# Optimization experiments

Measured on AMD Instinct MI355X. Metric: run time of the kernel, lower is better.

## Reference

```python
import jax, jax.numpy as jnp
import numpy as np

PAD_ID, SOS_ID, EOS_ID = 0, 1, 2


def setup_inputs() -> dict:
    key = jax.random.key(0)
    ks = jax.random.split(key, 8)
    V, E, H, B = 16000, 256, 512, 8
    s = 0.05  # weight scale to keep softmax well-conditioned
    return {
        "hidden": jax.random.normal(ks[0], (1, B, H), dtype=jnp.float32),
        "embedding": jax.random.normal(ks[1], (V, E), dtype=jnp.float32) * s,
        "w_ih": jax.random.normal(ks[2], (3 * H, E), dtype=jnp.float32) * s,
        "w_hh": jax.random.normal(ks[3], (3 * H, H), dtype=jnp.float32) * s,
        "b_ih": jax.random.normal(ks[4], (3 * H,), dtype=jnp.float32) * s,
        "b_hh": jax.random.normal(ks[5], (3 * H,), dtype=jnp.float32) * s,
        "w_out": jax.random.normal(ks[6], (V, H), dtype=jnp.float32) * s,
        "b_out": jax.random.normal(ks[7], (V,), dtype=jnp.float32) * s,
        "lenseq": 12,
        "k": 5,
    }


def reference(hidden, embedding, w_ih, w_hh, b_ih, b_hh, w_out, b_out, lenseq, k):
    V, E = embedding.shape
    _, B, H = hidden.shape
    dt = hidden.dtype
    pad_onehot = jax.nn.one_hot(PAD_ID, V, dtype=dt)

    def gru_cell(x_emb, h):  # x_emb: (k,B,E), h: (k,B,H); torch nn.GRU gate order r,z,n
        gi = x_emb @ w_ih.T + b_ih
        gh = h @ w_hh.T + b_hh
        i_r, i_z, i_n = jnp.split(gi, 3, axis=-1)
        h_r, h_z, h_n = jnp.split(gh, 3, axis=-1)
        r = jax.nn.sigmoid(i_r + h_r)
        z = jax.nn.sigmoid(i_z + h_z)
        n = jnp.tanh(i_n + r * h_n)
        return (1.0 - z) * n + z * h

    def step(carry, i):
        x, h, prob, res, _ = carry
        done = (x == EOS_ID) | (x == PAD_ID)            # (k,B)
        emb = embedding[x]                               # (k,B,E)
        h_new = gru_cell(emb, h)                         # (k,B,H)
        probs = jax.nn.softmax(h_new @ w_out.T + b_out, axis=-1)  # (k,B,V)
        pred = jnp.where(done[..., None], pad_onehot, probs)
        h = jnp.where(done[..., None], h, h_new)
        res = res.at[:, i].set(pred)                     # store raw pred (pre prob-scaling), as torch.cat copies
        scores = pred * prob[..., None]                  # (k,B,V); prob stays all-ones, faithful to source
        flat = scores.transpose(1, 0, 2).reshape(B, k * V)  # beam-major flatten per batch elem
        _, idx = jax.lax.top_k(flat, k)                  # (B,k)
        beam = (idx // V).T                              # (k,B)
        tok = (idx % V).T                                # (k,B)
        res = jnp.take_along_axis(res, beam[:, None, :, None], axis=0)
        prob = jnp.take_along_axis(prob, beam, axis=0)
        h = jnp.take_along_axis(h, beam[..., None], axis=0)
        return (tok, h, prob, res, pred), None

    x0 = jnp.full((k, B), SOS_ID, dtype=jnp.int32)
    h0 = jnp.broadcast_to(hidden[0], (k, B, H))
    prob0 = jnp.ones((k, B), dtype=dt)
    res0 = jnp.zeros((k, lenseq, B, V), dtype=dt)
    pred0 = jnp.zeros((k, B, V), dtype=dt)

    (x, h, prob, res, pred), _ = jax.lax.scan(step, (x0, h0, prob0, res0, pred0), jnp.arange(lenseq))

    # final top-1 selection per batch element over (k*V) flat scores
    scores = pred * prob[..., None]
    flat = scores.transpose(1, 0, 2).reshape(B, k * V)
    best_beam = jnp.argmax(flat, axis=-1) // V           # (B,)
    out = jnp.take_along_axis(res, best_beam[None, None, :, None], axis=0)[0]  # (lenseq,B,V)
    return out
```

## Files before the change

kernel.cpp:

```cpp
#include <hip/hip_runtime.h>

#define V 16000
#define E 256
#define H 512
#define HP 516
#define BB 8
#define T 12
#define NB 256
#define TPB 512
#define AGENT __HIP_MEMORY_SCOPE_AGENT


__device__ __forceinline__ float dot4(float4 a, float4 b) {
    return a.x * b.x + a.y * b.y + a.z * b.z + a.w * b.w;
}

__global__ __launch_bounds__(256) void kinit(const float* __restrict__ hidden,
                                             float* __restrict__ hA,
                                             int* __restrict__ cnt,
                                             int* __restrict__ flag) {
    int idx = blockIdx.x * 256 + threadIdx.x;
    if (idx < BB * H) hA[idx] = hidden[idx];
    if (idx < 64 * 16) cnt[idx] = 0;
    if (idx < 64) flag[idx] = 0;
}

__device__ __forceinline__ void stage_h(const float* __restrict__ g,
                                        float* __restrict__ s_h, int tid) {
    int r  = tid >> 6;
    int k0 = (tid & 63) * 8;
    const unsigned long long* p = (const unsigned long long*)(g + r * H + k0);
    float* d = s_h + r * HP + k0;
#pragma unroll
    for (int i = 0; i < 4; i++) {
        unsigned long long q = __hip_atomic_load(p + i, __ATOMIC_RELAXED, AGENT);
        union { unsigned long long u; float f[2]; } cv; cv.u = q;
        d[2 * i] = cv.f[0]; d[2 * i + 1] = cv.f[1];
    }
}

__device__ __forceinline__ void gridbar(int* __restrict__ cnt,
                                        int* __restrict__ flag, int ep) {
    __syncthreads();
    if (threadIdx.x == 0) {
        int g = blockIdx.x >> 2;
        int old = __hip_atomic_fetch_add(&cnt[g * 16], 1, __ATOMIC_RELEASE, AGENT);
        if (old == 4 * ep - 1)
            __hip_atomic_store(&flag[g], ep, __ATOMIC_RELAXED, AGENT);
    }
    if (threadIdx.x < 64) {
        while (!__all(__hip_atomic_load(&flag[threadIdx.x],
                                        __ATOMIC_RELAXED, AGENT) >= ep))
            __builtin_amdgcn_s_sleep(2);
    }
    __builtin_amdgcn_fence(__ATOMIC_ACQUIRE, "workgroup");
    __syncthreads();
}

__global__ __launch_bounds__(TPB) void kmain(
    const float* __restrict__ emb_tab,
    const float* __restrict__ w_ih,
    const float* __restrict__ w_hh,
    const float* __restrict__ b_ih,
    const float* __restrict__ b_hh,
    const float* __restrict__ w_out,
    const float* __restrict__ b_out,
    float* __restrict__ hA,
    float* __restrict__ hB,
    float* __restrict__ psum,
    float* __restrict__ pval,
    int* __restrict__ pidx,
    int* __restrict__ cnt,
    int* __restrict__ flag,
    float* __restrict__ out)
{
    const int blk = blockIdx.x, tid = threadIdx.x;

    __shared__ float s_h[BB * HP];
    __shared__ float s_part[64 * 48];
    __shared__ float s_v[TPB];
    __shared__ float s_av[TPB];
    __shared__ int   s_ai[TPB];
    __shared__ float s_S[BB];
    __shared__ int   s_Xn[BB];
    __shared__ int   s_X[BB];

    if (tid < BB) s_X[tid] = 1;
    __syncthreads();

    const int r  = tid & 7;
    const int vl = tid >> 3;
    const int v  = blk * 64 + vl;
    const bool ok = (v < V);
    float e = 0.f;

    for (int t = 0; t < T; t++) {
        const float* h_cur = (t & 1) ? hB : hA;
        float*       h_nxt = (t & 1) ? hA : hB;
        const int par = t & 1;

        if (blk < 64) {
            stage_h(h_cur, s_h, tid);
            __syncthreads();
            const int jl = tid >> 6;
            const int ar = (tid >> 3) & 7;
            const int kq = tid & 7;
            const int j  = blk * 8 + jl;
            const int pair = jl * 8 + ar;
            float gir = 0.f, giz = 0.f, gin = 0.f, ghr = 0.f, ghz = 0.f, ghn = 0.f;
            {
                const float* erow = emb_tab + (size_t)s_X[ar] * E;
                const float* w0 = w_ih + (size_t)j * E;
                const float* w1 = w0 + (size_t)H * E;
                const float* w2 = w1 + (size_t)H * E;
                const int k0 = kq * (E / 8);
                for (int k = k0; k < k0 + E / 8; k += 4) {
                    float4 ev = *(const float4*)(erow + k);
                    gir += dot4(*(const float4*)(w0 + k), ev);
                    giz += dot4(*(const float4*)(w1 + k), ev);
                    gin += dot4(*(const float4*)(w2 + k), ev);
                }
            }
            {
                const float* hrow = s_h + ar * HP;
                const float* w0 = w_hh + (size_t)j * H;
                const float* w1 = w0 + (size_t)H * H;
                const float* w2 = w1 + (size_t)H * H;
                const int k0 = kq * (H / 8);
                for (int k = k0; k < k0 + H / 8; k += 4) {
                    float4 hv = *(const float4*)(hrow + k);
                    ghr += dot4(*(const float4*)(w0 + k), hv);
                    ghz += dot4(*(const float4*)(w1 + k), hv);
                    ghn += dot4(*(const float4*)(w2 + k), hv);
                }
            }
            float* sp = s_part + pair * 48;
            sp[0 * 8 + kq] = gir; sp[1 * 8 + kq] = giz; sp[2 * 8 + kq] = gin;
            sp[3 * 8 + kq] = ghr; sp[4 * 8 + kq] = ghz; sp[5 * 8 + kq] = ghn;
            __syncthreads();
            if (kq == 0) {
                const float* sp2 = s_part + pair * 48;
                float G[6];
#pragma unroll
                for (int gg = 0; gg < 6; gg++) {
                    float s = 0.f;
#pragma unroll
                    for (int q = 0; q < 8; q++) s += sp2[gg * 8 + q];
                    G[gg] = s;
                }
                float ir  = G[0] + b_ih[j],         hr_ = G[3] + b_hh[j];
                float iz  = G[1] + b_ih[H + j],     hz  = G[4] + b_hh[H + j];
                float inn = G[2] + b_ih[2 * H + j], hn  = G[5] + b_hh[2 * H + j];
                float rg = 1.f / (1.f + __expf(-(ir + hr_)));
                float zg = 1.f / (1.f + __expf(-(iz + hz)));
                float ng = tanhf(inn + rg * hn);
                float ho = s_h[ar * HP + j];
                int xr = s_X[ar];
                bool dn = (xr == 0) || (xr == 2);
                float hv = dn ? ho : ((1.f - zg) * ng + zg * ho);
                __hip_atomic_store(&h_nxt[ar * H + j], hv, __ATOMIC_RELAXED, AGENT);
            }
        }
        gridbar(cnt, flag, 2 * t + 1);

        stage_h(h_nxt, s_h, tid);
        __syncthreads();
        {
            const float* w  = w_out + (size_t)(ok ? v : 0) * H;
            const float* hr = s_h + r * HP;
            float a0 = 0.f, a1 = 0.f, a2 = 0.f, a3 = 0.f;
            for (int k = 0; k < H; k += 16) {
                float4 w0 = *(const float4*)(w + k);
                float4 w1 = *(const float4*)(w + k + 4);
                float4 w2 = *(const float4*)(w + k + 8);
                float4 w3 = *(const float4*)(w + k + 12);
                float4 h0 = *(const float4*)(hr + k);
                float4 h1 = *(const float4*)(hr + k + 4);
                float4 h2 = *(const float4*)(hr + k + 8);
                float4 h3 = *(const float4*)(hr + k + 12);
                a0 += dot4(w0, h0); a1 += dot4(w1, h1);
                a2 += dot4(w2, h2); a3 += dot4(w3, h3);
            }
            e = __expf(a0 + a1 + a2 + a3 + (ok ? b_out[v] : 0.f));
            s_v[tid]  = ok ? e : 0.f;
            s_av[tid] = ok ? e : -1.f;
            s_ai[tid] = ok ? v : 0x7fffffff;
        }
        __syncthreads();
        for (int s = 256; s >= 8; s >>= 1) {
            if (tid < s) {
                s_v[tid] += s_v[tid + s];
                float ov = s_av[tid + s]; int oi = s_ai[tid + s];
                if (ov > s_av[tid] || (ov == s_av[tid] && oi < s_ai[tid])) {
                    s_av[tid] = ov; s_ai[tid] = oi;
                }
            }
            __syncthreads();
        }
        if (tid < 8) {
            int o = (par * 8 + tid) * NB + blk;
            __hip_atomic_store(&psum[o], s_v[tid],  __ATOMIC_RELAXED, AGENT);
            __hip_atomic_store(&pval[o], s_av[tid], __ATOMIC_RELAXED, AGENT);
            __hip_atomic_store(&pidx[o], s_ai[tid], __ATOMIC_RELAXED, AGENT);
        }
        gridbar(cnt, flag, 2 * t + 2);

        {
            const int rw = tid >> 6;
            const int lane = tid & 63;
            const int base = (par * 8 + rw) * NB;
            float s = 0.f, bv = -1.f; int bi = 0x7fffffff;
#pragma unroll
            for (int c = 0; c < 4; c++) {
                int o = base + lane + 64 * c;
                s += __hip_atomic_load(&psum[o], __ATOMIC_RELAXED, AGENT);
                float ov = __hip_atomic_load(&pval[o], __ATOMIC_RELAXED, AGENT);
                int   oi = __hip_atomic_load(&pidx[o], __ATOMIC_RELAXED, AGENT);
                if (ov > bv || (ov == bv && oi < bi)) { bv = ov; bi = oi; }
            }
            for (int m = 1; m < 64; m <<= 1) {
                s += __shfl_xor(s, m, 64);
                float ov = __shfl_xor(bv, m, 64);
                int   oi = __shfl_xor(bi, m, 64);
                if (ov > bv || (ov == bv && oi < bi)) { bv = ov; bi = oi; }
            }
            if (lane == 0) { s_S[rw] = s; s_Xn[rw] = bi; }
        }
        __syncthreads();
        {
            float* out_t = out + (size_t)t * BB * V;
            int xr = s_X[r];
            bool dn = (xr == 0) || (xr == 2);
            float inv = 1.f / s_S[r];
            if (ok) {
                float val = dn ? ((v == 0) ? 1.f : 0.f) : e * inv;
                __builtin_nontemporal_store(val, out_t + r * V + v);
            }
        }
        __syncthreads();
        if (tid < 8) {
            int xo = s_X[tid];
            s_X[tid] = ((xo == 0) || (xo == 2)) ? 0 : s_Xn[tid];
        }
        __syncthreads();
    }
}

extern "C" void kernel_launch(void* const* d_in, const int* in_sizes, int n_in,
                              void* d_out, int out_size, void* d_ws, size_t ws_size,
                              hipStream_t stream) {
    (void)in_sizes; (void)n_in; (void)out_size; (void)ws_size;
    const float* hidden    = (const float*)d_in[0];
    const float* embedding = (const float*)d_in[1];
    const float* w_ih      = (const float*)d_in[2];
    const float* w_hh      = (const float*)d_in[3];
    const float* b_ih      = (const float*)d_in[4];
    const float* b_hh      = (const float*)d_in[5];
    const float* w_out     = (const float*)d_in[6];
    const float* b_out     = (const float*)d_in[7];
    float* out = (float*)d_out;

    float* ws   = (float*)d_ws;
    float* hA   = ws;
    float* hB   = hA + BB * H;
    float* psum = hB + BB * H;
    float* pval = psum + 2 * 8 * NB;
    int*   pidx = (int*)(pval + 2 * 8 * NB);
    int*   cnt  = pidx + 2 * 8 * NB;
    int*   flag = cnt + 64 * 16;

    kinit<<<16, 256, 0, stream>>>(hidden, hA, cnt, flag);
    kmain<<<NB, TPB, 0, stream>>>(embedding, w_ih, w_hh, b_ih, b_hh, w_out, b_out,
                                  hA, hB, psum, pval, pidx, cnt, flag, out);
}
```

Baseline: 617.7 us.

## Use centralized epoch grid barrier and software-pipeline the output projection loads

Changes the grid barrier so that block 0 waits on the 64 leaf counters and then publishes one epoch word, which the other blocks poll with a single thread, replacing the 64-lane polling of per-group flags in every block. Fully unrolls the GRU gate dot-product loops and double-buffers the w_out row loads in registers so the next chunk is in flight while the current one is consumed. The barrier change cuts polling traffic but adds a serial hop through block 0, and the register double-buffering raises register pressure.

Result: slower. 2.432 ms (+293.7%).

```diff
diff --git a/kernel.cpp b/kernel.cpp
--- a/kernel.cpp
+++ b/kernel.cpp
@@ -17,12 +17,12 @@
 
 __global__ __launch_bounds__(256) void kinit(const float* __restrict__ hidden,
                                              float* __restrict__ hA,
-                                             int* __restrict__ cnt,
-                                             int* __restrict__ flag) {
+                                             int* __restrict__ leaf,
+                                             int* __restrict__ epoch) {
     int idx = blockIdx.x * 256 + threadIdx.x;
     if (idx < BB * H) hA[idx] = hidden[idx];
-    if (idx < 64 * 16) cnt[idx] = 0;
-    if (idx < 64) flag[idx] = 0;
+    if (idx < 64 * 16) leaf[idx] = 0;
+    if (idx == 0) epoch[0] = 0;
 }
 
 __device__ __forceinline__ void stage_h(const float* __restrict__ g,
@@ -39,19 +39,27 @@
     }
 }
 
-__device__ __forceinline__ void gridbar(int* __restrict__ cnt,
-                                        int* __restrict__ flag, int ep) {
+__device__ __forceinline__ void gridbar(int* __restrict__ leaf,
+                                        int* __restrict__ epoch, int ep) {
     __syncthreads();
     if (threadIdx.x == 0) {
         int g = blockIdx.x >> 2;
-        int old = __hip_atomic_fetch_add(&cnt[g * 16], 1, __ATOMIC_RELEASE, AGENT);
-        if (old == 4 * ep - 1)
-            __hip_atomic_store(&flag[g], ep, __ATOMIC_RELAXED, AGENT);
+        __hip_atomic_fetch_add(&leaf[g * 16], 1, __ATOMIC_RELEASE, AGENT);
     }
-    if (threadIdx.x < 64) {
-        while (!__all(__hip_atomic_load(&flag[threadIdx.x],
-                                        __ATOMIC_RELAXED, AGENT) >= ep))
-            __builtin_amdgcn_s_sleep(2);
+    if (blockIdx.x == 0) {
+        if (threadIdx.x < 64) {
+            while (__hip_atomic_load(&leaf[threadIdx.x * 16],
+                                     __ATOMIC_RELAXED, AGENT) < 4 * ep)
+                __builtin_amdgcn_s_sleep(1);
+        }
+        __syncthreads();
+        if (threadIdx.x == 0)
+            __hip_atomic_store(epoch, ep, __ATOMIC_RELAXED, AGENT);
+    } else {
+        if (threadIdx.x == 0) {
+            while (__hip_atomic_load(epoch, __ATOMIC_RELAXED, AGENT) < ep)
+                __builtin_amdgcn_s_sleep(1);
+        }
     }
     __builtin_amdgcn_fence(__ATOMIC_ACQUIRE, "workgroup");
     __syncthreads();
@@ -70,8 +78,8 @@
     float* __restrict__ psum,
     float* __restrict__ pval,
     int* __restrict__ pidx,
-    int* __restrict__ cnt,
-    int* __restrict__ flag,
+    int* __restrict__ leaf,
+    int* __restrict__ epoch,
     float* __restrict__ out)
 {
     const int blk = blockIdx.x, tid = threadIdx.x;
@@ -114,11 +122,12 @@
                 const float* w1 = w0 + (size_t)H * E;
                 const float* w2 = w1 + (size_t)H * E;
                 const int k0 = kq * (E / 8);
-                for (int k = k0; k < k0 + E / 8; k += 4) {
-                    float4 ev = *(const float4*)(erow + k);
-                    gir += dot4(*(const float4*)(w0 + k), ev);
-                    giz += dot4(*(const float4*)(w1 + k), ev);
-                    gin += dot4(*(const float4*)(w2 + k), ev);
+#pragma unroll
+                for (int k = 0; k < E / 8; k += 4) {
+                    float4 ev = *(const float4*)(erow + k0 + k);
+                    gir += dot4(*(const float4*)(w0 + k0 + k), ev);
+                    giz += dot4(*(const float4*)(w1 + k0 + k), ev);
+                    gin += dot4(*(const float4*)(w2 + k0 + k), ev);
                 }
             }
             {
@@ -127,11 +136,12 @@
                 const float* w1 = w0 + (size_t)H * H;
                 const float* w2 = w1 + (size_t)H * H;
                 const int k0 = kq * (H / 8);
-                for (int k = k0; k < k0 + H / 8; k += 4) {
-                    float4 hv = *(const float4*)(hrow + k);
-                    ghr += dot4(*(const float4*)(w0 + k), hv);
-                    ghz += dot4(*(const float4*)(w1 + k), hv);
-                    ghn += dot4(*(const float4*)(w2 + k), hv);
+#pragma unroll
+                for (int k = 0; k < H / 8; k += 4) {
+                    float4 hv = *(const float4*)(hrow + k0 + k);
+                    ghr += dot4(*(const float4*)(w0 + k0 + k), hv);
+                    ghz += dot4(*(const float4*)(w1 + k0 + k), hv);
+                    ghn += dot4(*(const float4*)(w2 + k0 + k), hv);
                 }
             }
             float* sp = s_part + pair * 48;
@@ -161,27 +171,47 @@
                 __hip_atomic_store(&h_nxt[ar * H + j], hv, __ATOMIC_RELAXED, AGENT);
             }
         }
-        gridbar(cnt, flag, 2 * t + 1);
+        gridbar(leaf, epoch, 2 * t + 1);
 
         stage_h(h_nxt, s_h, tid);
         __syncthreads();
         {
             const float* w  = w_out + (size_t)(ok ? v : 0) * H;
             const float* hr = s_h + r * HP;
+            float4 A0[8], A1[8];
             float a0 = 0.f, a1 = 0.f, a2 = 0.f, a3 = 0.f;
-            for (int k = 0; k < H; k += 16) {
-                float4 w0 = *(const float4*)(w + k);
-                float4 w1 = *(const float4*)(w + k + 4);
-                float4 w2 = *(const float4*)(w + k + 8);
-                float4 w3 = *(const float4*)(w + k + 12);
-                float4 h0 = *(const float4*)(hr + k);
-                float4 h1 = *(const float4*)(hr + k + 4);
-                float4 h2 = *(const float4*)(hr + k + 8);
-                float4 h3 = *(const float4*)(hr + k + 12);
-                a0 += dot4(w0, h0); a1 += dot4(w1, h1);
-                a2 += dot4(w2, h2); a3 += dot4(w3, h3);
-            }
-            e = __expf(a0 + a1 + a2 + a3 + (ok ? b_out[v] : 0.f));
+#pragma unroll
+            for (int i = 0; i < 8; i++) A0[i] = *(const float4*)(w + 4 * i);
+#pragma unroll
+            for (int c = 0; c < 16; c += 2) {
+#pragma unroll
+                for (int i = 0; i < 8; i++)
+                    A1[i] = *(const float4*)(w + (c + 1) * 32 + 4 * i);
+#pragma unroll
+                for (int i = 0; i < 8; i++) {
+                    float4 h4 = *(const float4*)(hr + c * 32 + 4 * i);
+                    float d = dot4(A0[i], h4);
+                    if (i == 0 || i == 4) a0 += d;
+                    else if (i == 1 || i == 5) a1 += d;
+                    else if (i == 2 || i == 6) a2 += d;
+                    else a3 += d;
+                }
+                if (c + 2 < 16) {
+#pragma unroll
+                    for (int i = 0; i < 8; i++)
+                        A0[i] = *(const float4*)(w + (c + 2) * 32 + 4 * i);
+                }
+#pragma unroll
+                for (int i = 0; i < 8; i++) {
+                    float4 h4 = *(const float4*)(hr + (c + 1) * 32 + 4 * i);
+                    float d = dot4(A1[i], h4);
+                    if (i == 0 || i == 4) a0 += d;
+                    else if (i == 1 || i == 5) a1 += d;
+                    else if (i == 2 || i == 6) a2 += d;
+                    else a3 += d;
+                }
+            }
+            e = __expf((a0 + a1) + (a2 + a3) + (ok ? b_out[v] : 0.f));
             s_v[tid]  = ok ? e : 0.f;
             s_av[tid] = ok ? e : -1.f;
             s_ai[tid] = ok ? v : 0x7fffffff;
@@ -203,7 +233,7 @@
             __hip_atomic_store(&pval[o], s_av[tid], __ATOMIC_RELAXED, AGENT);
             __hip_atomic_store(&pidx[o], s_ai[tid], __ATOMIC_RELAXED, AGENT);
         }
-        gridbar(cnt, flag, 2 * t + 2);
+        gridbar(leaf, epoch, 2 * t + 2);
 
         {
             const int rw = tid >> 6;
@@ -260,16 +290,16 @@
     const float* b_out     = (const float*)d_in[7];
     float* out = (float*)d_out;
 
-    float* ws   = (float*)d_ws;
-    float* hA   = ws;
-    float* hB   = hA + BB * H;
-    float* psum = hB + BB * H;
-    float* pval = psum + 2 * 8 * NB;
-    int*   pidx = (int*)(pval + 2 * 8 * NB);
-    int*   cnt  = pidx + 2 * 8 * NB;
-    int*   flag = cnt + 64 * 16;
-
-    kinit<<<16, 256, 0, stream>>>(hidden, hA, cnt, flag);
+    float* ws    = (float*)d_ws;
+    float* hA    = ws;
+    float* hB    = hA + BB * H;
+    float* psum  = hB + BB * H;
+    float* pval  = psum + 2 * 8 * NB;
+    int*   pidx  = (int*)(pval + 2 * 8 * NB);
+    int*   leaf  = pidx + 2 * 8 * NB;
+    int*   epoch = leaf + 64 * 16;
+
+    kinit<<<16, 256, 0, stream>>>(hidden, hA, leaf, epoch);
     kmain<<<NB, TPB, 0, stream>>>(embedding, w_ih, w_hh, b_ih, b_hh, w_out, b_out,
-                                  hA, hB, psum, pval, pidx, cnt, flag, out);
-}
+                                  hA, hB, psum, pval, pidx, leaf, epoch, out);
+}
```
